# Performance work log

Measured on AMD Instinct MI355X. Metric: run time of the kernel, lower is better.

Reference implementation:

```python
import jax, jax.numpy as jnp
import numpy as np

DIM = 512
QK_DIM = 128
HIDDEN = 2 * DIM  # expansion_factor * dim
EPS = 1e-5


def layernorm(x, scale, bias):
    mu = jnp.mean(x, axis=-1, keepdims=True)
    var = jnp.mean((x - mu) ** 2, axis=-1, keepdims=True)
    return (x - mu) * jax.lax.rsqrt(var + EPS) * scale + bias


def setup_inputs() -> dict:
    key = jax.random.key(0)
    ks = jax.random.split(key, 8)
    b, s = 4, 4096
    x = jax.random.normal(ks[0], (b, s, DIM), dtype=jnp.float32)
    inv = lambda fan_in: 1.0 / np.sqrt(fan_in)
    W_hidden = jax.random.normal(ks[1], (DIM, 2 * HIDDEN), dtype=jnp.float32) * inv(DIM)
    b_hidden = jnp.zeros((2 * HIDDEN,), dtype=jnp.float32)
    W_qk = jax.random.normal(ks[2], (DIM, QK_DIM), dtype=jnp.float32) * inv(DIM)
    b_qk = jnp.zeros((QK_DIM,), dtype=jnp.float32)
    gamma = jax.random.normal(ks[3], (2, QK_DIM), dtype=jnp.float32) * 0.02
    beta = jnp.zeros((2, QK_DIM), dtype=jnp.float32)
    W_out = jax.random.normal(ks[4], (HIDDEN, DIM), dtype=jnp.float32) * inv(HIDDEN)
    b_out = jnp.zeros((DIM,), dtype=jnp.float32)
    norm_scale = jnp.ones((DIM,), dtype=jnp.float32)
    norm_bias = jnp.zeros((DIM,), dtype=jnp.float32)
    return {
        "x": x,
        "norm_scale": norm_scale,
        "norm_bias": norm_bias,
        "W_hidden": W_hidden,
        "b_hidden": b_hidden,
        "W_qk": W_qk,
        "b_qk": b_qk,
        "gamma": gamma,
        "beta": beta,
        "W_out": W_out,
        "b_out": b_out,
    }


def reference(x, norm_scale, norm_bias, W_hidden, b_hidden, W_qk, b_qk, gamma, beta, W_out, b_out):
    seq_len = x.shape[-2]
    normed = layernorm(x, norm_scale, norm_bias)
    hidden = jax.nn.silu(normed @ W_hidden + b_hidden)          # [b, s, 2*hidden]
    v, gate = jnp.split(hidden, 2, axis=-1)                      # each [b, s, hidden]
    Z = jax.nn.silu(normed @ W_qk + b_qk)                        # [b, s, qk]
    QK = Z[..., None, :] * gamma + beta                          # [b, s, 2, qk]
    q = QK[..., 0, :]
    k = QK[..., 1, :]
    sim = jnp.einsum('bid,bjd->bij', q, k) / seq_len             # [b, s, s]
    A = jnp.square(jax.nn.relu(sim))
    V = jnp.einsum('bij,bjd->bid', A, v) * gate                  # [b, s, hidden]
    out = V @ W_out + b_out
    return out + x
```

## Files before the change

kernel.cpp:

```cpp
#include <hip/hip_runtime.h>
#include <cstdint>
#include <cstddef>

#define DIM   512
#define QKD   128
#define HID   1024
#define SEQ   4096
#define BAT   4
#define TOK   (BAT*SEQ)

typedef float f32x4 __attribute__((ext_vector_type(4)));
typedef int   i32x4 __attribute__((ext_vector_type(4)));
typedef int   i32x8 __attribute__((ext_vector_type(8)));

__device__ __forceinline__ float silu_f(float x) { return x / (1.f + __expf(-x)); }

__device__ __forceinline__ unsigned char f2e4(float f) {
    int v = __builtin_amdgcn_cvt_pk_fp8_f32(f, 0.f, 0, false);
    return (unsigned char)(v & 0xff);
}
__device__ __forceinline__ unsigned f2e4x4(float a, float b, float c, float d) {
    int w = __builtin_amdgcn_cvt_pk_fp8_f32(a, b, 0, false);
    w = __builtin_amdgcn_cvt_pk_fp8_f32(c, d, w, true);
    return (unsigned)w;
}
__device__ __forceinline__ float e42f(unsigned char b) {
    return __builtin_amdgcn_cvt_f32_fp8((int)b, 0);
}

__device__ __forceinline__ void load16_lds(const void* gp, void* lp) {
    __builtin_amdgcn_global_load_lds(
        (const __attribute__((address_space(1))) unsigned int*)gp,
        (__attribute__((address_space(3))) unsigned int*)lp,
        16, 0, 0);
}

#define WAITV8() asm volatile("s_waitcnt vmcnt(8)" ::: "memory")
#define WAITV6() asm volatile("s_waitcnt vmcnt(6)" ::: "memory")
#define WAITV0() asm volatile("s_waitcnt vmcnt(0)" ::: "memory")
#define FENCE()  do { asm volatile("" ::: "memory"); __builtin_amdgcn_sched_barrier(0); } while (0)

__global__ __launch_bounds__(256) void ln_kernel(
    const float* __restrict__ x, const float* __restrict__ sc,
    const float* __restrict__ bi, unsigned char* __restrict__ out)
{
    const int lane = threadIdx.x & 63, wid = threadIdx.x >> 6;
    const int row  = blockIdx.x * 4 + wid;
    const float4* xr = (const float4*)(x + (size_t)row * DIM);
    float4 a = xr[lane], b = xr[64 + lane];
    float s = a.x + a.y + a.z + a.w + b.x + b.y + b.z + b.w;
    float q = a.x*a.x + a.y*a.y + a.z*a.z + a.w*a.w
            + b.x*b.x + b.y*b.y + b.z*b.z + b.w*b.w;
#pragma unroll
    for (int m = 1; m < 64; m <<= 1) { s += __shfl_xor(s, m); q += __shfl_xor(q, m); }
    const float mean = s * (1.f / DIM);
    const float var  = q * (1.f / DIM) - mean * mean;
    const float rs   = rsqrtf(var + 1e-5f);
    float4 s0 = ((const float4*)sc)[lane], s1 = ((const float4*)sc)[64 + lane];
    float4 b0 = ((const float4*)bi)[lane], b1 = ((const float4*)bi)[64 + lane];
    unsigned wlo = f2e4x4((a.x - mean) * rs * s0.x + b0.x,
                          (a.y - mean) * rs * s0.y + b0.y,
                          (a.z - mean) * rs * s0.z + b0.z,
                          (a.w - mean) * rs * s0.w + b0.w);
    unsigned whi = f2e4x4((b.x - mean) * rs * s1.x + b1.x,
                          (b.y - mean) * rs * s1.y + b1.y,
                          (b.z - mean) * rs * s1.z + b1.z,
                          (b.w - mean) * rs * s1.w + b1.w);
    unsigned char* orow = out + (size_t)row * DIM;
    *(unsigned*)(orow + 4 * lane)       = wlo;
    *(unsigned*)(orow + 256 + 4 * lane) = whi;
}

__global__ __launch_bounds__(256) void tcast_f2e4_kernel(
    const float* __restrict__ in, unsigned char* __restrict__ out, int R, int C)
{
    __shared__ float t[32][33];
    const int tx = threadIdx.x & 31, ty = threadIdx.x >> 5;
    const int c0 = blockIdx.x * 32, r0 = blockIdx.y * 32;
#pragma unroll
    for (int i = 0; i < 4; ++i)
        t[ty + i * 8][tx] = in[(size_t)(r0 + ty + i * 8) * C + c0 + tx];
    __syncthreads();
#pragma unroll
    for (int i = 0; i < 4; ++i)
        out[(size_t)(c0 + ty + i * 8) * R + r0 + tx] = f2e4(t[tx][ty + i * 8] * 16.f);
}

__global__ __launch_bounds__(256) void copy_kernel(
    const float* __restrict__ in, float* __restrict__ out, int n4)
{
    int i = blockIdx.x * 256 + threadIdx.x;
    int stride = gridDim.x * 256;
    for (; i < n4; i += stride)
        ((float4*)out)[i] = ((const float4*)in)[i];
}

template<int EPI, int NX>
__global__ __launch_bounds__(256) void gemm8(
    const unsigned char* __restrict__ A, const unsigned char* __restrict__ B,
    int K, long strAz, long strBz, long strOz,
    const float* __restrict__ f0, const float* __restrict__ f1,
    const float* __restrict__ f2, const float* __restrict__ f3,
    const float* __restrict__ f4, const float* __restrict__ f5,
    unsigned char* __restrict__ gate,
    unsigned char* __restrict__ o0, unsigned char* __restrict__ o1,
    unsigned char* __restrict__ o2,
    float* __restrict__ fo, float scale)
{
    __shared__ unsigned char lds[32768];
    const int tid = threadIdx.x;
    const int d  = blockIdx.x + NX * blockIdx.y;
    const int qd = d >> 3;
    const int m0 = ((d & 7) + 8 * (qd / NX)) * 128;
    const int n0 = (qd % NX) * 128;
    const int z  = blockIdx.z;
    A += (size_t)z * strAz;  B += (size_t)z * strBz;
    const int lane = tid & 63, wid = tid >> 6;
    const int wm   = (wid & 1) * 64, wn = (wid >> 1) * 64;
    const int l15  = lane & 15, quad = lane >> 4;

    f32x4 acc[4][4] = {};

    const int srow = tid >> 3, sseg = tid & 7;
    const int gseg = sseg ^ (srow & 7);
    const unsigned char* gA = A + (size_t)(m0 + srow) * K + gseg * 16;
    const unsigned char* gB = B + (size_t)(n0 + srow) * K + gseg * 16;
    unsigned char* lA = lds + (size_t)tid * 16;
    unsigned char* lB = lds + 16384 + (size_t)tid * 16;

    const int olo = (((quad << 1) ^ (l15 & 7)) << 4);
    const int ohi = olo ^ 16;

    for (int kt = 0; kt < K; kt += 128) {
#pragma unroll
        for (int i = 0; i < 4; ++i)
            load16_lds(gA + (size_t)i * 32 * K + kt, lA + i * 4096);
#pragma unroll
        for (int i = 0; i < 4; ++i)
            load16_lds(gB + (size_t)i * 32 * K + kt, lB + i * 4096);
        __syncthreads();
        i32x4 alo[4], ahi[4], blo[4], bhi[4];
#pragma unroll
        for (int mi = 0; mi < 4; ++mi) {
            const unsigned char* p = lds + (wm + mi * 16 + l15) * 128;
            alo[mi] = *(const i32x4*)(p + olo); ahi[mi] = *(const i32x4*)(p + ohi);
        }
#pragma unroll
        for (int ni = 0; ni < 4; ++ni) {
            const unsigned char* p = lds + 16384 + (wn + ni * 16 + l15) * 128;
            blo[ni] = *(const i32x4*)(p + olo); bhi[ni] = *(const i32x4*)(p + ohi);
        }
#pragma unroll
        for (int mi = 0; mi < 4; ++mi) {
            i32x8 af = __builtin_shufflevector(alo[mi], ahi[mi], 0,1,2,3,4,5,6,7);
#pragma unroll
            for (int ni = 0; ni < 4; ++ni) {
                i32x8 bf = __builtin_shufflevector(blo[ni], bhi[ni], 0,1,2,3,4,5,6,7);
                acc[mi][ni] = __builtin_amdgcn_mfma_scale_f32_16x16x128_f8f6f4(
                    af, bf, acc[mi][ni], 0, 0,
                    0, 0x7F7F7F7F, 0, 0x7F7F7F7F);
            }
        }
        __syncthreads();
    }

#pragma unroll
    for (int mi = 0; mi < 4; ++mi)
#pragma unroll
    for (int ni = 0; ni < 4; ++ni) {
        const int grow0 = m0 + wm + mi * 16 + quad * 4;
        const int gcol  = n0 + wn + ni * 16 + l15;
        if constexpr (EPI == 1) {
            unsigned char* Ao = o0 + (size_t)z * strOz;
#pragma unroll
            for (int r = 0; r < 4; ++r) {
                float t = fmaxf(acc[mi][ni][r], 0.f) * 0.0625f;
                Ao[(size_t)(grow0 + r) * SEQ + gcol] = f2e4(t * t);
            }
        }
    }
}

template<int EPI, int NX>
__global__ __launch_bounds__(512, 2) void gemm8p(
    const unsigned char* __restrict__ A, const unsigned char* __restrict__ B,
    int K, long strAz, long strBz, long strOz,
    const float* __restrict__ f0, const float* __restrict__ f1,
    const float* __restrict__ f2, const float* __restrict__ f3,
    const float* __restrict__ f4, const float* __restrict__ f5,
    unsigned char* __restrict__ gate,
    unsigned char* __restrict__ o0, unsigned char* __restrict__ o1,
    unsigned char* __restrict__ o2,
    float* __restrict__ fo, float scale)
{
    __shared__ unsigned char lds[3 * 49152];
    const int tid = threadIdx.x;
    const int d  = blockIdx.x + NX * blockIdx.y;
    const int qd = d >> 3;
    const int m0 = ((d & 7) + 8 * (qd / NX)) * 256;
    const int n0 = (qd % NX) * 128;
    const int z  = blockIdx.z;
    A += (size_t)z * strAz;  B += (size_t)z * strBz;
    const int lane = tid & 63, wid = tid >> 6;
    const int wm   = (wid & 3) * 64, wn = (wid >> 2) * 64;
    const int l15  = lane & 15, quad = lane >> 4;

    f32x4 acc[4][4] = {};

    const int srow = tid >> 3, sseg = tid & 7;
    const int gseg = sseg ^ (srow & 7);
    const unsigned char* gAs = A + (size_t)(m0 + srow) * K + gseg * 16;
    const unsigned char* gBs = B + (size_t)(n0 + srow) * K + gseg * 16;

    const int olo = (((quad << 1) ^ (l15 & 7)) << 4);
    const int ohi = olo ^ 16;

    const int NT = K >> 7;

    auto STAGE = [&](int t, int buf) {
        const size_t ko = (size_t)t << 7;
        unsigned char* lb = lds + buf * 49152 + tid * 16;
#pragma unroll
        for (int i = 0; i < 4; ++i)
            load16_lds(gAs + (size_t)(i * 64) * K + ko, lb + i * 8192);
#pragma unroll
        for (int i = 0; i < 2; ++i)
            load16_lds(gBs + (size_t)(i * 64) * K + ko, lb + 32768 + i * 8192);
    };

    auto COMPUTE = [&](int buf) {
        const unsigned char* la = lds + buf * 49152;
        const unsigned char* lb = la + 32768;
        i32x4 alo[4], ahi[4], blo[4], bhi[4];
#pragma unroll
        for (int mi = 0; mi < 4; ++mi) {
            const unsigned char* p = la + (size_t)(wm + mi * 16 + l15) * 128;
            alo[mi] = *(const i32x4*)(p + olo); ahi[mi] = *(const i32x4*)(p + ohi);
        }
#pragma unroll
        for (int ni = 0; ni < 4; ++ni) {
            const unsigned char* p = lb + (size_t)(wn + ni * 16 + l15) * 128;
            blo[ni] = *(const i32x4*)(p + olo); bhi[ni] = *(const i32x4*)(p + ohi);
        }
#pragma unroll
        for (int mi = 0; mi < 4; ++mi) {
            i32x8 af = __builtin_shufflevector(alo[mi], ahi[mi], 0,1,2,3,4,5,6,7);
#pragma unroll
            for (int ni = 0; ni < 4; ++ni) {
                i32x8 bf = __builtin_shufflevector(blo[ni], bhi[ni], 0,1,2,3,4,5,6,7);
                acc[mi][ni] = __builtin_amdgcn_mfma_scale_f32_16x16x128_f8f6f4(
                    af, bf, acc[mi][ni], 0, 0,
                    0, 0x7F7F7F7F, 0, 0x7F7F7F7F);
            }
        }
    };

    STAGE(0, 0);
    if (NT > 1) { STAGE(1, 1); WAITV6(); }
    else        {              WAITV0(); }
    __builtin_amdgcn_s_barrier();
    FENCE();

    int cbuf = 0, sbuf = 2;
    for (int t = 0; t < NT; ++t) {
        if (t + 2 < NT) STAGE(t + 2, sbuf);
        COMPUTE(cbuf);
        if (t + 1 < NT) {
            if (t + 2 < NT) WAITV6(); else WAITV0();
            __builtin_amdgcn_s_barrier();
            FENCE();
        }
        cbuf = (cbuf == 2) ? 0 : cbuf + 1;
        sbuf = (sbuf == 2) ? 0 : sbuf + 1;
    }

#pragma unroll
    for (int mi = 0; mi < 4; ++mi)
#pragma unroll
    for (int ni = 0; ni < 4; ++ni) {
        const int grow0 = m0 + wm + mi * 16 + quad * 4;
        const int gcol  = n0 + wn + ni * 16 + l15;
        if constexpr (EPI == 0) {
            if (gcol < HID) {
                const int b = grow0 >> 12, rloc = grow0 & (SEQ - 1);
                unsigned w = f2e4x4(silu_f(acc[mi][ni][0] * 0.0625f + f0[gcol]),
                                    silu_f(acc[mi][ni][1] * 0.0625f + f0[gcol]),
                                    silu_f(acc[mi][ni][2] * 0.0625f + f0[gcol]),
                                    silu_f(acc[mi][ni][3] * 0.0625f + f0[gcol]));
                *(unsigned*)(o0 + (size_t)b * HID * SEQ + (size_t)gcol * SEQ + rloc) = w;
            } else if (gcol < 2048) {
#pragma unroll
                for (int r = 0; r < 4; ++r)
                    gate[(size_t)(grow0 + r) * HID + (gcol - HID)] =
                        f2e4(silu_f(acc[mi][ni][r] * 0.0625f + f0[gcol]));
            } else {
                const int c = gcol - 2048;
#pragma unroll
                for (int r = 0; r < 4; ++r) {
                    float zf = silu_f(acc[mi][ni][r] * 0.0625f + f1[c]);
                    o1[(size_t)(grow0 + r) * QKD + c] = f2e4((zf * f2[c] + f4[c]) * 64.f);
                    o2[(size_t)(grow0 + r) * QKD + c] = f2e4((zf * f3[c] + f5[c]) * 64.f);
                }
            }
        } else if constexpr (EPI == 2) {
            unsigned char* gz = gate + (size_t)z * strOz;
            unsigned char* vo = o0 + (size_t)z * strOz;
#pragma unroll
            for (int r = 0; r < 4; ++r) {
                float g = e42f(gz[(size_t)(grow0 + r) * HID + gcol]);
                vo[(size_t)(grow0 + r) * HID + gcol] = f2e4(acc[mi][ni][r] * scale * g);
            }
        } else if constexpr (EPI == 3) {
#pragma unroll
            for (int r = 0; r < 4; ++r)
                fo[(size_t)(grow0 + r) * DIM + gcol] =
                    acc[mi][ni][r] * scale + f0[gcol] + f1[(size_t)(grow0 + r) * DIM + gcol];
        }
    }
}

template<int EPI, int NX>
__global__ __launch_bounds__(512, 2) void gemm9p(
    const unsigned char* __restrict__ A, const unsigned char* __restrict__ B,
    int K, long strAz, long strBz, long strOz,
    unsigned char* __restrict__ gate,
    unsigned char* __restrict__ o0, float scale)
{
    __shared__ unsigned char lds[2 * 65536];
    const int tid = threadIdx.x;
    const int d  = blockIdx.x + NX * blockIdx.y;
    const int qd = d >> 3;
    const int m0 = ((d & 7) + 8 * (qd / NX)) * 256;
    const int n0 = (qd % NX) * 256;
    const int z  = blockIdx.z;
    A += (size_t)z * strAz;  B += (size_t)z * strBz;
    const int lane = tid & 63, wid = tid >> 6;
    const int wm   = (wid & 1) * 128, wn = (wid >> 1) * 64;
    const int l15  = lane & 15, quad = lane >> 4;

    f32x4 acc[8][4] = {};

    const int srow = tid >> 3, sseg = tid & 7;
    const int gseg = sseg ^ (srow & 7);
    const unsigned char* gAs = A + (size_t)(m0 + srow) * K + gseg * 16;
    const unsigned char* gBs = B + (size_t)(n0 + srow) * K + gseg * 16;

    const int olo = (((quad << 1) ^ (l15 & 7)) << 4);
    const int ohi = olo ^ 16;

    const int NT = K >> 7;

    auto STAGE = [&](int t, int buf) {
        const size_t ko = (size_t)t << 7;
        unsigned char* lb = lds + buf * 65536 + tid * 16;
#pragma unroll
        for (int i = 0; i < 4; ++i)
            load16_lds(gAs + (size_t)(i * 64) * K + ko, lb + i * 8192);
#pragma unroll
        for (int i = 0; i < 4; ++i)
            load16_lds(gBs + (size_t)(i * 64) * K + ko, lb + 32768 + i * 8192);
    };

    auto COMPUTE = [&](int buf) {
        const unsigned char* la = lds + buf * 65536;
        const unsigned char* lb = la + 32768;
        i32x8 bf[4];
#pragma unroll
        for (int ni = 0; ni < 4; ++ni) {
            const unsigned char* p = lb + (size_t)(wn + ni * 16 + l15) * 128;
            i32x4 lo = *(const i32x4*)(p + olo), hi = *(const i32x4*)(p + ohi);
            bf[ni] = __builtin_shufflevector(lo, hi, 0,1,2,3,4,5,6,7);
        }
#pragma unroll
        for (int mi = 0; mi < 8; ++mi) {
            const unsigned char* p = la + (size_t)(wm + mi * 16 + l15) * 128;
            i32x4 lo = *(const i32x4*)(p + olo), hi = *(const i32x4*)(p + ohi);
            i32x8 af = __builtin_shufflevector(lo, hi, 0,1,2,3,4,5,6,7);
#pragma unroll
            for (int ni = 0; ni < 4; ++ni)
                acc[mi][ni] = __builtin_amdgcn_mfma_scale_f32_16x16x128_f8f6f4(
                    af, bf[ni], acc[mi][ni], 0, 0,
                    0, 0x7F7F7F7F, 0, 0x7F7F7F7F);
        }
    };

    STAGE(0, 0);
    for (int t = 0; t < NT; ++t) {
        const int cb = t & 1;
        if (t + 1 < NT) { STAGE(t + 1, cb ^ 1); WAITV8(); }
        else            {                       WAITV0(); }
        __builtin_amdgcn_s_barrier();
        FENCE();
        COMPUTE(cb);
        if (t + 1 < NT) {
            __builtin_amdgcn_s_barrier();
            FENCE();
        }
    }

#pragma unroll
    for (int mi = 0; mi < 8; ++mi)
#pragma unroll
    for (int ni = 0; ni < 4; ++ni) {
        const int grow0 = m0 + wm + mi * 16 + quad * 4;
        const int gcol  = n0 + wn + ni * 16 + l15;
        if constexpr (EPI == 2) {
            unsigned char* gz = gate + (size_t)z * strOz;
            unsigned char* vo = o0 + (size_t)z * strOz;
#pragma unroll
            for (int r = 0; r < 4; ++r) {
                float g = e42f(gz[(size_t)(grow0 + r) * HID + gcol]);
                vo[(size_t)(grow0 + r) * HID + gcol] = f2e4(acc[mi][ni][r] * scale * g);
            }
        }
    }
}

extern "C" void kernel_launch(void* const* d_in, const int* in_sizes, int n_in,
                              void* d_out, int out_size, void* d_ws, size_t ws_size,
                              hipStream_t stream) {
    const float* x     = (const float*)d_in[0];
    const float* nsc   = (const float*)d_in[1];
    const float* nbi   = (const float*)d_in[2];
    const float* Wh    = (const float*)d_in[3];
    const float* bh    = (const float*)d_in[4];
    const float* Wqk   = (const float*)d_in[5];
    const float* bqk   = (const float*)d_in[6];
    const float* gamma = (const float*)d_in[7];
    const float* beta  = (const float*)d_in[8];
    const float* Wout  = (const float*)d_in[9];
    const float* bout  = (const float*)d_in[10];
    float* out = (float*)d_out;

    uint8_t* ws = (uint8_t*)d_ws;
    size_t off = 0;
    auto alloc = [&](size_t n) { uint8_t* p = ws + off; off += (n + 255) & ~(size_t)255; return p; };
    unsigned char* normed8 = (unsigned char*)alloc((size_t)TOK * DIM);
    unsigned char* Wc8     = (unsigned char*)alloc((size_t)2176 * DIM);
    unsigned char* Wout8   = (unsigned char*)alloc((size_t)DIM * HID);
    unsigned char* vT8     = (unsigned char*)alloc((size_t)BAT * HID * SEQ);
    unsigned char* gbuf    = (unsigned char*)alloc((size_t)TOK * HID);
    unsigned char* q8      = (unsigned char*)alloc((size_t)TOK * QKD);
    unsigned char* k8      = (unsigned char*)alloc((size_t)TOK * QKD);
    unsigned char* Ab8     = (unsigned char*)alloc((size_t)BAT * SEQ * SEQ);
    unsigned char* vg8     = (unsigned char*)alloc((size_t)TOK * HID);

    if (ws_size < off) {
        copy_kernel<<<4096, 256, 0, stream>>>(x, out, TOK * DIM / 4);
        return;
    }

    ln_kernel<<<TOK / 4, 256, 0, stream>>>(x, nsc, nbi, normed8);
    tcast_f2e4_kernel<<<dim3(2048 / 32, DIM / 32), 256, 0, stream>>>(Wh, Wc8, DIM, 2048);
    tcast_f2e4_kernel<<<dim3(QKD / 32, DIM / 32), 256, 0, stream>>>(
        Wqk, Wc8 + (size_t)2048 * DIM, DIM, QKD);
    tcast_f2e4_kernel<<<dim3(DIM / 32, HID / 32), 256, 0, stream>>>(Wout, Wout8, HID, DIM);

    gemm8p<0, 17><<<dim3(17, TOK / 256), 512, 0, stream>>>(
        normed8, Wc8, DIM, 0, 0, 0,
        bh, bqk, gamma, gamma + QKD, beta, beta + QKD,
        gbuf, vT8, q8, k8, nullptr, 0.f);

    gemm8<1, 32><<<dim3(SEQ / 128, SEQ / 128, BAT), 256, 0, stream>>>(
        q8, k8, QKD, (long)SEQ * QKD, (long)SEQ * QKD, (long)SEQ * SEQ,
        nullptr, nullptr, nullptr, nullptr, nullptr, nullptr,
        nullptr, Ab8, nullptr, nullptr, nullptr, 0.f);

    gemm9p<2, 4><<<dim3(HID / 256, SEQ / 256, BAT), 512, 0, stream>>>(
        Ab8, vT8, SEQ, (long)SEQ * SEQ, (long)HID * SEQ, (long)SEQ * HID,
        gbuf, vg8, 0x1p-12f);

    gemm8p<3, 4><<<dim3(DIM / 128, TOK / 256), 512, 0, stream>>>(
        vg8, Wout8, HID, 0, 0, 0,
        bout, x, nullptr, nullptr, nullptr, nullptr,
        nullptr, nullptr, nullptr, nullptr, out, 0x1p-32f);
}
```

Measured before the change: 282.6 us.

## Interleave LDS fragment loads with MFMA phases using barriers and priority

Splits each K-tile compute of both FP8 GEMM kernels into phases of two A-row fragments. Each phase loads its fragments, crosses a workgroup barrier, waits on lgkmcnt, and runs its MFMAs at raised wave priority. The aim is to have waves alternate between LDS reads and matrix math so that load latency and compute overlap across waves, in a ping-pong style. The cost is several extra barriers per tile, and waves may stall on each other if the phases are unbalanced.

```diff
diff --git a/kernel.cpp b/kernel.cpp
--- a/kernel.cpp
+++ b/kernel.cpp
@@ -39,6 +39,7 @@
 #define WAITV6() asm volatile("s_waitcnt vmcnt(6)" ::: "memory")
 #define WAITV0() asm volatile("s_waitcnt vmcnt(0)" ::: "memory")
 #define FENCE()  do { asm volatile("" ::: "memory"); __builtin_amdgcn_sched_barrier(0); } while (0)
+#define LGKM0()  do { asm volatile("s_waitcnt lgkmcnt(0)" ::: "memory"); __builtin_amdgcn_sched_barrier(0); } while (0)
 
 __global__ __launch_bounds__(256) void ln_kernel(
     const float* __restrict__ x, const float* __restrict__ sc,
@@ -228,33 +229,6 @@
             load16_lds(gBs + (size_t)(i * 64) * K + ko, lb + 32768 + i * 8192);
     };
 
-    auto COMPUTE = [&](int buf) {
-        const unsigned char* la = lds + buf * 49152;
-        const unsigned char* lb = la + 32768;
-        i32x4 alo[4], ahi[4], blo[4], bhi[4];
-#pragma unroll
-        for (int mi = 0; mi < 4; ++mi) {
-            const unsigned char* p = la + (size_t)(wm + mi * 16 + l15) * 128;
-            alo[mi] = *(const i32x4*)(p + olo); ahi[mi] = *(const i32x4*)(p + ohi);
-        }
-#pragma unroll
-        for (int ni = 0; ni < 4; ++ni) {
-            const unsigned char* p = lb + (size_t)(wn + ni * 16 + l15) * 128;
-            blo[ni] = *(const i32x4*)(p + olo); bhi[ni] = *(const i32x4*)(p + ohi);
-        }
-#pragma unroll
-        for (int mi = 0; mi < 4; ++mi) {
-            i32x8 af = __builtin_shufflevector(alo[mi], ahi[mi], 0,1,2,3,4,5,6,7);
-#pragma unroll
-            for (int ni = 0; ni < 4; ++ni) {
-                i32x8 bf = __builtin_shufflevector(blo[ni], bhi[ni], 0,1,2,3,4,5,6,7);
-                acc[mi][ni] = __builtin_amdgcn_mfma_scale_f32_16x16x128_f8f6f4(
-                    af, bf, acc[mi][ni], 0, 0,
-                    0, 0x7F7F7F7F, 0, 0x7F7F7F7F);
-            }
-        }
-    };
-
     STAGE(0, 0);
     if (NT > 1) { STAGE(1, 1); WAITV6(); }
     else        {              WAITV0(); }
@@ -264,7 +238,39 @@
     int cbuf = 0, sbuf = 2;
     for (int t = 0; t < NT; ++t) {
         if (t + 2 < NT) STAGE(t + 2, sbuf);
-        COMPUTE(cbuf);
+        const unsigned char* la = lds + cbuf * 49152;
+        const unsigned char* lb = la + 32768;
+        i32x8 bf[4];
+#pragma unroll
+        for (int ni = 0; ni < 4; ++ni) {
+            const unsigned char* p = lb + (size_t)(wn + ni * 16 + l15) * 128;
+            i32x4 lo = *(const i32x4*)(p + olo), hi = *(const i32x4*)(p + ohi);
+            bf[ni] = __builtin_shufflevector(lo, hi, 0,1,2,3,4,5,6,7);
+        }
+#pragma unroll
+        for (int ph = 0; ph < 2; ++ph) {
+            i32x8 af0, af1;
+            {
+                const unsigned char* p0 = la + (size_t)(wm + (ph * 2)     * 16 + l15) * 128;
+                const unsigned char* p1 = la + (size_t)(wm + (ph * 2 + 1) * 16 + l15) * 128;
+                i32x4 lo0 = *(const i32x4*)(p0 + olo), hi0 = *(const i32x4*)(p0 + ohi);
+                i32x4 lo1 = *(const i32x4*)(p1 + olo), hi1 = *(const i32x4*)(p1 + ohi);
+                af0 = __builtin_shufflevector(lo0, hi0, 0,1,2,3,4,5,6,7);
+                af1 = __builtin_shufflevector(lo1, hi1, 0,1,2,3,4,5,6,7);
+            }
+            __builtin_amdgcn_s_barrier();
+            LGKM0();
+            __builtin_amdgcn_s_setprio(1);
+#pragma unroll
+            for (int ni = 0; ni < 4; ++ni) {
+                acc[ph * 2][ni] = __builtin_amdgcn_mfma_scale_f32_16x16x128_f8f6f4(
+                    af0, bf[ni], acc[ph * 2][ni], 0, 0, 0, 0x7F7F7F7F, 0, 0x7F7F7F7F);
+                acc[ph * 2 + 1][ni] = __builtin_amdgcn_mfma_scale_f32_16x16x128_f8f6f4(
+                    af1, bf[ni], acc[ph * 2 + 1][ni], 0, 0, 0, 0x7F7F7F7F, 0, 0x7F7F7F7F);
+            }
+            __builtin_amdgcn_s_setprio(0);
+            if (ph == 0) __builtin_amdgcn_s_barrier();
+        }
         if (t + 1 < NT) {
             if (t + 2 < NT) WAITV6(); else WAITV0();
             __builtin_amdgcn_s_barrier();
@@ -361,29 +367,6 @@
             load16_lds(gBs + (size_t)(i * 64) * K + ko, lb + 32768 + i * 8192);
     };
 
-    auto COMPUTE = [&](int buf) {
-        const unsigned char* la = lds + buf * 65536;
-        const unsigned char* lb = la + 32768;
-        i32x8 bf[4];
-#pragma unroll
-        for (int ni = 0; ni < 4; ++ni) {
-            const unsigned char* p = lb + (size_t)(wn + ni * 16 + l15) * 128;
-            i32x4 lo = *(const i32x4*)(p + olo), hi = *(const i32x4*)(p + ohi);
-            bf[ni] = __builtin_shufflevector(lo, hi, 0,1,2,3,4,5,6,7);
-        }
-#pragma unroll
-        for (int mi = 0; mi < 8; ++mi) {
-            const unsigned char* p = la + (size_t)(wm + mi * 16 + l15) * 128;
-            i32x4 lo = *(const i32x4*)(p + olo), hi = *(const i32x4*)(p + ohi);
-            i32x8 af = __builtin_shufflevector(lo, hi, 0,1,2,3,4,5,6,7);
-#pragma unroll
-            for (int ni = 0; ni < 4; ++ni)
-                acc[mi][ni] = __builtin_amdgcn_mfma_scale_f32_16x16x128_f8f6f4(
-                    af, bf[ni], acc[mi][ni], 0, 0,
-                    0, 0x7F7F7F7F, 0, 0x7F7F7F7F);
-        }
-    };
-
     STAGE(0, 0);
     for (int t = 0; t < NT; ++t) {
         const int cb = t & 1;
@@ -391,10 +374,38 @@
         else            {                       WAITV0(); }
         __builtin_amdgcn_s_barrier();
         FENCE();
-        COMPUTE(cb);
-        if (t + 1 < NT) {
+        const unsigned char* la = lds + cb * 65536;
+        const unsigned char* lb = la + 32768;
+        i32x8 bf[4];
+#pragma unroll
+        for (int ni = 0; ni < 4; ++ni) {
+            const unsigned char* p = lb + (size_t)(wn + ni * 16 + l15) * 128;
+            i32x4 lo = *(const i32x4*)(p + olo), hi = *(const i32x4*)(p + ohi);
+            bf[ni] = __builtin_shufflevector(lo, hi, 0,1,2,3,4,5,6,7);
+        }
+#pragma unroll
+        for (int ph = 0; ph < 4; ++ph) {
+            i32x8 af0, af1;
+            {
+                const unsigned char* p0 = la + (size_t)(wm + (ph * 2)     * 16 + l15) * 128;
+                const unsigned char* p1 = la + (size_t)(wm + (ph * 2 + 1) * 16 + l15) * 128;
+                i32x4 lo0 = *(const i32x4*)(p0 + olo), hi0 = *(const i32x4*)(p0 + ohi);
+                i32x4 lo1 = *(const i32x4*)(p1 + olo), hi1 = *(const i32x4*)(p1 + ohi);
+                af0 = __builtin_shufflevector(lo0, hi0, 0,1,2,3,4,5,6,7);
+                af1 = __builtin_shufflevector(lo1, hi1, 0,1,2,3,4,5,6,7);
+            }
             __builtin_amdgcn_s_barrier();
-            FENCE();
+            LGKM0();
+            __builtin_amdgcn_s_setprio(1);
+#pragma unroll
+            for (int ni = 0; ni < 4; ++ni) {
+                acc[ph * 2][ni] = __builtin_amdgcn_mfma_scale_f32_16x16x128_f8f6f4(
+                    af0, bf[ni], acc[ph * 2][ni], 0, 0, 0, 0x7F7F7F7F, 0, 0x7F7F7F7F);
+                acc[ph * 2 + 1][ni] = __builtin_amdgcn_mfma_scale_f32_16x16x128_f8f6f4(
+                    af1, bf[ni], acc[ph * 2 + 1][ni], 0, 0, 0, 0x7F7F7F7F, 0, 0x7F7F7F7F);
+            }
+            __builtin_amdgcn_s_setprio(0);
+            __builtin_amdgcn_s_barrier();
         }
     }
 
```

After: 290.4 us. +2.8%, slower.

## Load B fragments directly into registers and halve LDS in fp8 GEMM

Applied to the files above, without the earlier changes.

The gemm9p kernel no longer stages the B tile through LDS. Each wave reads its 32-byte B fragments straight from global memory into registers, double-buffered across two register sets in a loop unrolled by two. Only A still goes through LDS, which halves shared memory per block and cuts LDS read traffic. The cost is that two waves now fetch the same B rows redundantly from global memory or L2. Global-load latency is also exposed more directly, and every step does a full __syncthreads wait instead of the earlier partial vmcnt wait.

```diff
diff --git a/kernel.cpp b/kernel.cpp
--- a/kernel.cpp
+++ b/kernel.cpp
@@ -35,10 +35,9 @@
         16, 0, 0);
 }
 
-#define WAITV8() asm volatile("s_waitcnt vmcnt(8)" ::: "memory")
-#define WAITV6() asm volatile("s_waitcnt vmcnt(6)" ::: "memory")
-#define WAITV0() asm volatile("s_waitcnt vmcnt(0)" ::: "memory")
-#define FENCE()  do { asm volatile("" ::: "memory"); __builtin_amdgcn_sched_barrier(0); } while (0)
+#define WAITV6()  asm volatile("s_waitcnt vmcnt(6)" ::: "memory")
+#define WAITV0()  asm volatile("s_waitcnt vmcnt(0)" ::: "memory")
+#define FENCE()   do { asm volatile("" ::: "memory"); __builtin_amdgcn_sched_barrier(0); } while (0)
 
 __global__ __launch_bounds__(256) void ln_kernel(
     const float* __restrict__ x, const float* __restrict__ sc,
@@ -326,7 +325,7 @@
     unsigned char* __restrict__ gate,
     unsigned char* __restrict__ o0, float scale)
 {
-    __shared__ unsigned char lds[2 * 65536];
+    __shared__ unsigned char lds[2 * 32768];
     const int tid = threadIdx.x;
     const int d  = blockIdx.x + NX * blockIdx.y;
     const int qd = d >> 3;
@@ -343,34 +342,27 @@
     const int srow = tid >> 3, sseg = tid & 7;
     const int gseg = sseg ^ (srow & 7);
     const unsigned char* gAs = A + (size_t)(m0 + srow) * K + gseg * 16;
-    const unsigned char* gBs = B + (size_t)(n0 + srow) * K + gseg * 16;
 
     const int olo = (((quad << 1) ^ (l15 & 7)) << 4);
     const int ohi = olo ^ 16;
 
+    const unsigned char* gBf = B + (size_t)(n0 + wn + l15) * K + quad * 32;
+
     const int NT = K >> 7;
 
-    auto STAGE = [&](int t, int buf) {
-        const size_t ko = (size_t)t << 7;
-        unsigned char* lb = lds + buf * 65536 + tid * 16;
+    auto STAGEA = [&](int t, int buf) {
+        unsigned char* lb = lds + buf * 32768 + tid * 16;
 #pragma unroll
         for (int i = 0; i < 4; ++i)
-            load16_lds(gAs + (size_t)(i * 64) * K + ko, lb + i * 8192);
-#pragma unroll
-        for (int i = 0; i < 4; ++i)
-            load16_lds(gBs + (size_t)(i * 64) * K + ko, lb + 32768 + i * 8192);
+            load16_lds(gAs + (size_t)(i * 64) * K + ((size_t)t << 7), lb + i * 8192);
     };
-
-    auto COMPUTE = [&](int buf) {
-        const unsigned char* la = lds + buf * 65536;
-        const unsigned char* lb = la + 32768;
-        i32x8 bf[4];
-#pragma unroll
-        for (int ni = 0; ni < 4; ++ni) {
-            const unsigned char* p = lb + (size_t)(wn + ni * 16 + l15) * 128;
-            i32x4 lo = *(const i32x4*)(p + olo), hi = *(const i32x4*)(p + ohi);
-            bf[ni] = __builtin_shufflevector(lo, hi, 0,1,2,3,4,5,6,7);
-        }
+    auto LOADB = [&](i32x8* bf, int t) {
+#pragma unroll
+        for (int ni = 0; ni < 4; ++ni)
+            bf[ni] = *(const i32x8*)(gBf + (size_t)(ni * 16) * K + ((size_t)t << 7));
+    };
+    auto COMPUTE = [&](const i32x8* bf, int buf) {
+        const unsigned char* la = lds + buf * 32768;
 #pragma unroll
         for (int mi = 0; mi < 8; ++mi) {
             const unsigned char* p = la + (size_t)(wm + mi * 16 + l15) * 128;
@@ -384,18 +376,18 @@
         }
     };
 
-    STAGE(0, 0);
-    for (int t = 0; t < NT; ++t) {
-        const int cb = t & 1;
-        if (t + 1 < NT) { STAGE(t + 1, cb ^ 1); WAITV8(); }
-        else            {                       WAITV0(); }
-        __builtin_amdgcn_s_barrier();
-        FENCE();
-        COMPUTE(cb);
-        if (t + 1 < NT) {
-            __builtin_amdgcn_s_barrier();
-            FENCE();
-        }
+    i32x8 bfA[4], bfB[4];
+    STAGEA(0, 0);
+    LOADB(bfA, 0);
+    __syncthreads();
+
+    for (int t2 = 0; t2 < NT; t2 += 2) {
+        if (t2 + 1 < NT) { STAGEA(t2 + 1, 1); LOADB(bfB, t2 + 1); FENCE(); }
+        COMPUTE(bfA, 0);
+        __syncthreads();
+        if (t2 + 2 < NT) { STAGEA(t2 + 2, 0); LOADB(bfA, t2 + 2); FENCE(); }
+        COMPUTE(bfB, 1);
+        __syncthreads();
     }
 
 #pragma unroll
```

New measurement: 476.9 us. 68.7% more time.
